# Optimization experiments

Hardware: AMD Instinct MI355X
Metric: run time of the kernel (lower is better)

The kernel has to match this reference:

```python
import jax, jax.numpy as jnp
import numpy as np

B, S, D = 2, 2048, 768
E, TOP_K = 8, 2
H = 4 * D  # expert hidden dim


def setup_inputs() -> dict:
    key = jax.random.key(0)
    ks = jax.random.split(key, 8)
    s_in = 1.0 / np.sqrt(D)
    s_h = 1.0 / np.sqrt(H)
    return {
        "x": jax.random.normal(ks[0], (B, S, D), dtype=jnp.float32),
        "gate_w": jax.random.uniform(ks[1], (D, E), jnp.float32, -s_in, s_in),
        "gate_b": jax.random.uniform(ks[2], (E,), jnp.float32, -s_in, s_in),
        "w1": jax.random.uniform(ks[3], (E, D, H), jnp.float32, -s_in, s_in),
        "b1": jax.random.uniform(ks[4], (E, H), jnp.float32, -s_in, s_in),
        "w2": jax.random.uniform(ks[5], (E, H, D), jnp.float32, -s_h, s_h),
        "b2": jax.random.uniform(ks[6], (E, D), jnp.float32, -s_h, s_h),
    }


def reference(x, gate_w, gate_b, w1, b1, w2, b2):
    # Router: gate linear -> top-k -> softmax over the k selected logits
    logits = jnp.einsum("bsd,de->bse", x, gate_w) + gate_b          # [B,S,E]
    top_vals, top_idx = jax.lax.top_k(logits, TOP_K)                 # [B,S,K]
    rw = jax.nn.softmax(top_vals, axis=-1)                           # [B,S,K]
    # Per-token per-expert combine weight (0 for unselected experts)
    onehot = jax.nn.one_hot(top_idx, E, dtype=x.dtype)               # [B,S,K,E]
    expert_w = jnp.einsum("bske,bsk->bse", onehot, rw)               # [B,S,E]

    # Expert MLPs (GELU exact, matching torch nn.GELU default; dropout is
    # identity in eval). Stacked as grouped GEMMs over the expert axis.
    h = jax.nn.gelu(jnp.einsum("bsd,edh->bseh", x, w1) + b1, approximate=False)
    y = jnp.einsum("bseh,ehd->bsed", h, w2) + b2                     # [B,S,E,D]
    # Weighted combine over experts
    return jnp.einsum("bse,bsed->bsd", expert_w, y)                  # [B,S,D]
```

## Files before the change

### kernel.cpp

```cpp
#include <hip/hip_runtime.h>
#include <hip/hip_bf16.h>

#define D_ 768
#define E_ 8
#define H_ 3072
#define N_TOK 4096
#define BT 64
#define BK 64

typedef _Float16 f16;
typedef f16 f16x8 __attribute__((ext_vector_type(8)));
typedef float f32x4 __attribute__((ext_vector_type(4)));

__device__ __forceinline__ void gld16(const f16* g, f16* l) {
    __builtin_amdgcn_global_load_lds(
        (const __attribute__((address_space(1))) unsigned int*)g,
        (__attribute__((address_space(3))) unsigned int*)l, 16, 0, 0);
}

#define TP 66
__global__ __launch_bounds__(256) void cvt_w_t(const float* __restrict__ in,
                                               f16* __restrict__ outp,
                                               int R, int C) {
    __shared__ f16 t[64][TP];
    const float* src = in + (size_t)blockIdx.z * R * C;
    f16* dst = outp + (size_t)blockIdx.z * R * C;
    int r0 = blockIdx.y * 64, c0 = blockIdx.x * 64;
    int tid = threadIdx.x;
    {
        int r = tid >> 4;
        int c = (tid & 15) * 4;
#pragma unroll
        for (int i = 0; i < 4; i++) {
            float4 v = *(const float4*)(src + (size_t)(r0 + r + i * 16) * C + (c0 + c));
            t[r + i * 16][c] = (f16)v.x;
            t[r + i * 16][c + 1] = (f16)v.y;
            t[r + i * 16][c + 2] = (f16)v.z;
            t[r + i * 16][c + 3] = (f16)v.w;
        }
    }
    __syncthreads();
    {
        int c = tid >> 3;
        int rr = (tid & 7) * 8;
        int ch = rr >> 3;
#pragma unroll
        for (int i = 0; i < 2; i++) {
            int cc = c + i * 32;
            int rowi = c0 + cc;
            f16x8 o;
#pragma unroll
            for (int j = 0; j < 8; j++) o[j] = t[rr + j][cc];
            *(f16x8*)(dst + (size_t)rowi * R + r0 + (((ch ^ rowi) & 7) << 3)) = o;
        }
    }
}

__global__ __launch_bounds__(1024) void router(const float* __restrict__ x,
                                               const float* __restrict__ gw,
                                               const float* __restrict__ gb,
                                               int* __restrict__ counts,
                                               int* __restrict__ list,
                                               float* __restrict__ wslot) {
    __shared__ int lcount[E_];
    __shared__ int lbase[E_];
    __shared__ int te0[64], te1[64], ts0[64], ts1[64];
    __shared__ float tw0[64], tw1[64];

    int tid = threadIdx.x;
    int wv = tid >> 6, lane = tid & 63;
    int s = lane >> 3, eL = lane & 7;
    if (tid < E_) lcount[tid] = 0;
    __syncthreads();

    float biasL = gb[eL];

#pragma unroll 1
    for (int i = 0; i < 4; i++) {
        int lt = wv * 4 + i;
        int tok = blockIdx.x * 64 + lt;
        const float* xr = x + (size_t)tok * D_;
        float a = 0.f;
        const float* gwl = gw + lane;
#pragma unroll 8
        for (int j = 0; j < 96; j++)
            a = fmaf(xr[j * 8 + s], gwl[j * 64], a);
        a += __shfl_xor(a, 8, 64);
        a += __shfl_xor(a, 16, 64);
        a += __shfl_xor(a, 32, 64);
        float lg = a + biasL;
        float le[8];
#pragma unroll
        for (int q = 0; q < 8; q++) le[q] = __shfl(lg, q, 64);
        float v0 = -3.4e38f, v1 = -3.4e38f;
        int i0 = 0, i1 = 0;
#pragma unroll
        for (int q = 0; q < 8; q++) {
            float l = le[q];
            if (l > v0) { v1 = v0; i1 = i0; v0 = l; i0 = q; }
            else if (l > v1) { v1 = l; i1 = q; }
        }
        if (lane == 0) {
            float p1 = expf(v1 - v0);
            float ssum = 1.f + p1;
            int s0 = atomicAdd(&lcount[i0], 1);
            int s1 = atomicAdd(&lcount[i1], 1);
            te0[lt] = i0; ts0[lt] = s0; tw0[lt] = 1.f / ssum;
            te1[lt] = i1; ts1[lt] = s1; tw1[lt] = p1 / ssum;
        }
    }
    __syncthreads();
    if (tid < E_) lbase[tid] = atomicAdd(&counts[tid], lcount[tid]);
    __syncthreads();
    if (tid < 64) {
        int tok = blockIdx.x * 64 + tid;
        int e0 = te0[tid], e1 = te1[tid];
        list[e0 * N_TOK + lbase[e0] + ts0[tid]] = tok * 2;
        list[e1 * N_TOK + lbase[e1] + ts1[tid]] = tok * 2 + 1;
        wslot[tok * 2] = tw0[tid];
        wslot[tok * 2 + 1] = tw1[tid];
    }
}

__global__ void scan8(const int* __restrict__ counts, int* __restrict__ offs) {
    if (threadIdx.x == 0) {
        int s = 0;
#pragma unroll
        for (int e = 0; e < E_; e++) { offs[e] = s; s += counts[e]; }
        offs[E_] = s;
    }
}

__global__ __launch_bounds__(256) void pack_a(const float* __restrict__ x,
                                              const int* __restrict__ counts,
                                              const int* __restrict__ offs,
                                              const int* __restrict__ list,
                                              f16* __restrict__ xg) {
    int wv = threadIdx.x >> 6, lane = threadIdx.x & 63;
    int idx = blockIdx.x * 4 + wv;
    int e = idx >> 12, j = idx & (N_TOK - 1);
    if (j >= counts[e]) return;
    int id = list[idx];
    int row = offs[e] + j;
    const float* xr = x + (size_t)(id >> 1) * D_;
    f16* dst = xg + (size_t)row * D_;
    int r7 = row & 7;
#pragma unroll
    for (int c = 0; c < 3; c++) {
        int h = lane * 4 + c * 256;
        float4 v = *(const float4*)(xr + h);
        f16 o[4] = {(f16)v.x, (f16)v.y, (f16)v.z, (f16)v.w};
        int hs = (h & ~0x3F) | ((((h >> 3) ^ r7) & 7) << 3) | (h & 7);
        *(float2*)(dst + hs) = *(const float2*)o;
    }
}

#define NXB1 (H_ / BT)
__global__ __launch_bounds__(256, 8) void gemm1(const f16* __restrict__ xg,
                                                const f16* __restrict__ w1t,
                                                const float* __restrict__ b1,
                                                const int* __restrict__ counts,
                                                const int* __restrict__ offs,
                                                f16* __restrict__ hbuf) {
    int bid = blockIdx.x;
    int e = bid & 7;
    int r = bid >> 3;
    int xb = r % NXB1;
    int yb = r / NXB1;
    int cnt = counts[e];
    int off = offs[e];
    int rb = yb * BT;
    if (rb >= cnt) return;
    int cb = xb * BT;

    __shared__ f16 lds[2 * BT * BK];
    char* ldsb = (char*)lds;

    int tid = threadIdx.x;
    int wv = tid >> 6, lane = tid & 63;
    int lr = lane >> 3, lc = lane & 7;

    int r0l = wv * 8 + lr;
    int r1l = 32 + wv * 8 + lr;
    int ag0 = off + rb + r0l; if (ag0 > 8191) ag0 = 8191;
    int ag1 = off + rb + r1l; if (ag1 > 8191) ag1 = 8191;
    const f16* ap0 = xg + (size_t)ag0 * D_ + lc * 8;
    const f16* ap1 = xg + (size_t)ag1 * D_ + lc * 8;
    const f16* wb = w1t + (size_t)e * H_ * D_;
    const f16* bp0 = wb + (size_t)(cb + r0l) * D_ + lc * 8;
    const f16* bp1 = wb + (size_t)(cb + r1l) * D_ + lc * 8;
    f16* la0 = lds + wv * 512;
    f16* la1 = lds + 2048 + wv * 512;
    f16* lb0 = lds + 4096 + wv * 512;
    f16* lb1 = lds + 6144 + wv * 512;

    int wr = (wv >> 1) * 32, wc = (wv & 1) * 32;
    int fr = lane & 15, qh = lane >> 4;
    int koff = (off + rb) & 7;

    int roA[2][2], roB[2][2];
#pragma unroll
    for (int m = 0; m < 2; m++)
#pragma unroll
        for (int ks = 0; ks < 2; ks++) {
            int row = wr + m * 16 + fr;
            roA[m][ks] = row * 128 + ((((ks * 4 + qh) ^ (koff + row)) & 7) << 4);
            int rwb = wc + m * 16 + fr;
            roB[m][ks] = 8192 + rwb * 128 + ((((ks * 4 + qh) ^ rwb) & 7) << 4);
        }

    f32x4 acc[2][2] = {};
    const int NT = D_ / BK;
#pragma unroll 1
    for (int t = 0; t < NT; ++t) {
        int kk = t * BK;
        gld16(ap0 + kk, la0);
        gld16(ap1 + kk, la1);
        gld16(bp0 + kk, lb0);
        gld16(bp1 + kk, lb1);
        __syncthreads();
#pragma unroll
        for (int ks = 0; ks < 2; ks++) {
            f16x8 a0 = *(const f16x8*)(ldsb + roA[0][ks]);
            f16x8 a1 = *(const f16x8*)(ldsb + roA[1][ks]);
            f16x8 b0 = *(const f16x8*)(ldsb + roB[0][ks]);
            f16x8 b1v = *(const f16x8*)(ldsb + roB[1][ks]);
            acc[0][0] = __builtin_amdgcn_mfma_f32_16x16x32_f16(a0, b0, acc[0][0], 0, 0, 0);
            acc[0][1] = __builtin_amdgcn_mfma_f32_16x16x32_f16(a0, b1v, acc[0][1], 0, 0, 0);
            acc[1][0] = __builtin_amdgcn_mfma_f32_16x16x32_f16(a1, b0, acc[1][0], 0, 0, 0);
            acc[1][1] = __builtin_amdgcn_mfma_f32_16x16x32_f16(a1, b1v, acc[1][1], 0, 0, 0);
        }
        __syncthreads();
    }

#pragma unroll
    for (int n = 0; n < 2; n++) {
        int colg = cb + wc + n * 16 + fr;
        float bias = b1[e * H_ + colg];
#pragma unroll
        for (int m = 0; m < 2; m++) {
#pragma unroll
            for (int r2 = 0; r2 < 4; r2++) {
                int j = rb + wr + m * 16 + qh * 4 + r2;
                if (j < cnt) {
                    float v = acc[m][n][r2] + bias;
                    v = 0.5f * v * (1.f + erff(v * 0.70710678f));
                    int row = off + j;
                    int hs = (colg & ~0x3F) | ((((colg >> 3) ^ row) & 7) << 3) | (colg & 7);
                    hbuf[(size_t)row * H_ + hs] = (f16)v;
                }
            }
        }
    }
}

#define KSPLIT 2
#define KCH (H_ / KSPLIT)
#define NXB2 ((D_ / BT) * KSPLIT)
__global__ __launch_bounds__(256, 8) void gemm2(const f16* __restrict__ hbuf,
                                                const f16* __restrict__ w2t,
                                                const float* __restrict__ b2,
                                                const int* __restrict__ counts,
                                                const int* __restrict__ offs,
                                                const int* __restrict__ list,
                                                const float* __restrict__ wslot,
                                                float* __restrict__ out) {
    int bid = blockIdx.x;
    int e = bid & 7;
    int r = bid >> 3;
    int xk = r % NXB2;
    int yb = r / NXB2;
    int cnt = counts[e];
    int off = offs[e];
    int rb = yb * BT;
    if (rb >= cnt) return;
    int cb = (xk % (D_ / BT)) * BT;
    int kz = xk / (D_ / BT);
    int k0 = kz * KCH;

    __shared__ f16 lds[2 * BT * BK];
    char* ldsb = (char*)lds;

    int tid = threadIdx.x;
    int wv = tid >> 6, lane = tid & 63;
    int lr = lane >> 3, lc = lane & 7;

    int r0l = wv * 8 + lr;
    int r1l = 32 + wv * 8 + lr;
    int ag0 = off + rb + r0l; if (ag0 > 8191) ag0 = 8191;
    int ag1 = off + rb + r1l; if (ag1 > 8191) ag1 = 8191;
    const f16* ap0 = hbuf + (size_t)ag0 * H_ + k0 + lc * 8;
    const f16* ap1 = hbuf + (size_t)ag1 * H_ + k0 + lc * 8;
    const f16* wb = w2t + (size_t)e * D_ * H_;
    const f16* bp0 = wb + (size_t)(cb + r0l) * H_ + k0 + lc * 8;
    const f16* bp1 = wb + (size_t)(cb + r1l) * H_ + k0 + lc * 8;
    f16* la0 = lds + wv * 512;
    f16* la1 = lds + 2048 + wv * 512;
    f16* lb0 = lds + 4096 + wv * 512;
    f16* lb1 = lds + 6144 + wv * 512;

    int wr = (wv >> 1) * 32, wc = (wv & 1) * 32;
    int fr = lane & 15, qh = lane >> 4;
    int koff = (off + rb) & 7;

    int roA[2][2], roB[2][2];
#pragma unroll
    for (int m = 0; m < 2; m++)
#pragma unroll
        for (int ks = 0; ks < 2; ks++) {
            int row = wr + m * 16 + fr;
            roA[m][ks] = row * 128 + ((((ks * 4 + qh) ^ (koff + row)) & 7) << 4);
            int rwb = wc + m * 16 + fr;
            roB[m][ks] = 8192 + rwb * 128 + ((((ks * 4 + qh) ^ rwb) & 7) << 4);
        }

    f32x4 acc[2][2] = {};
    const int NT = KCH / BK;
#pragma unroll 1
    for (int t = 0; t < NT; ++t) {
        int kk = t * BK;
        gld16(ap0 + kk, la0);
        gld16(ap1 + kk, la1);
        gld16(bp0 + kk, lb0);
        gld16(bp1 + kk, lb1);
        __syncthreads();
#pragma unroll
        for (int ks = 0; ks < 2; ks++) {
            f16x8 a0 = *(const f16x8*)(ldsb + roA[0][ks]);
            f16x8 a1 = *(const f16x8*)(ldsb + roA[1][ks]);
            f16x8 b0 = *(const f16x8*)(ldsb + roB[0][ks]);
            f16x8 b1v = *(const f16x8*)(ldsb + roB[1][ks]);
            acc[0][0] = __builtin_amdgcn_mfma_f32_16x16x32_f16(a0, b0, acc[0][0], 0, 0, 0);
            acc[0][1] = __builtin_amdgcn_mfma_f32_16x16x32_f16(a0, b1v, acc[0][1], 0, 0, 0);
            acc[1][0] = __builtin_amdgcn_mfma_f32_16x16x32_f16(a1, b0, acc[1][0], 0, 0, 0);
            acc[1][1] = __builtin_amdgcn_mfma_f32_16x16x32_f16(a1, b1v, acc[1][1], 0, 0, 0);
        }
        __syncthreads();
    }

#pragma unroll
    for (int n = 0; n < 2; n++) {
        int colg = cb + wc + n * 16 + fr;
        float bias = (kz == 0) ? b2[e * D_ + colg] : 0.f;
#pragma unroll
        for (int m = 0; m < 2; m++) {
#pragma unroll
            for (int r2 = 0; r2 < 4; r2++) {
                int j = rb + wr + m * 16 + qh * 4 + r2;
                if (j < cnt) {
                    int id = list[e * N_TOK + j];
                    float w = wslot[id];
                    float v = (acc[m][n][r2] + bias) * w;
                    atomicAdd(&out[(size_t)(id >> 1) * D_ + colg], v);
                }
            }
        }
    }
}

extern "C" void kernel_launch(void* const* d_in, const int* in_sizes, int n_in,
                              void* d_out, int out_size, void* d_ws, size_t ws_size,
                              hipStream_t stream) {
    const float* x = (const float*)d_in[0];
    const float* gate_w = (const float*)d_in[1];
    const float* gate_b = (const float*)d_in[2];
    const float* w1 = (const float*)d_in[3];
    const float* b1 = (const float*)d_in[4];
    const float* w2 = (const float*)d_in[5];
    const float* b2 = (const float*)d_in[6];
    float* out = (float*)d_out;

    char* ws = (char*)d_ws;
    int* counts = (int*)ws;
    int* offs = (int*)(ws + 256);
    int* list = (int*)(ws + 1024);
    float* wslot = (float*)(ws + 132096);
    f16* xg = (f16*)(ws + 196608);
    f16* w1t = (f16*)(ws + 12779520);
    f16* w2t = (f16*)(ws + 50528256);
    f16* hbuf = (f16*)(ws + 88276992);

    hipMemsetAsync(counts, 0, 256, stream);
    hipMemsetAsync(out, 0, (size_t)out_size * sizeof(float), stream);

    router<<<64, 1024, 0, stream>>>(x, gate_w, gate_b, counts, list, wslot);
    scan8<<<1, 64, 0, stream>>>(counts, offs);
    pack_a<<<E_ * N_TOK / 4, 256, 0, stream>>>(x, counts, offs, list, xg);
    cvt_w_t<<<dim3(H_ / 64, D_ / 64, E_), 256, 0, stream>>>(w1, w1t, D_, H_);
    cvt_w_t<<<dim3(D_ / 64, H_ / 64, E_), 256, 0, stream>>>(w2, w2t, H_, D_);
    gemm1<<<E_ * NXB1 * (N_TOK / BT), 256, 0, stream>>>(xg, w1t, b1, counts, offs, hbuf);
    gemm2<<<E_ * NXB2 * (N_TOK / BT), 256, 0, stream>>>(hbuf, w2t, b2, counts, offs, list, wslot, out);
}
```

Baseline: 263.3 us.

## Drop scan kernel, merge weight conversions, reorder GEMM block grid

Removes the single-thread scan8 launch by having each kernel compute its expert's offset inline from the counts array. The two weight transpose/convert launches are merged into one kernel that picks w1 or w2 by blockIdx.z. The GEMM block-index decomposition is reordered so consecutive blocks share column tiles across row blocks, which may improve weight-tile cache reuse. Together these cut launch count and serialization gaps, at the cost of a small redundant prefix sum in every block.

```diff
diff --git a/kernel.cpp b/kernel.cpp
--- a/kernel.cpp
+++ b/kernel.cpp
@@ -18,14 +18,34 @@
         (__attribute__((address_space(3))) unsigned int*)l, 16, 0, 0);
 }
 
-#define TP 66
-__global__ __launch_bounds__(256) void cvt_w_t(const float* __restrict__ in,
-                                               f16* __restrict__ outp,
-                                               int R, int C) {
-    __shared__ f16 t[64][TP];
-    const float* src = in + (size_t)blockIdx.z * R * C;
-    f16* dst = outp + (size_t)blockIdx.z * R * C;
-    int r0 = blockIdx.y * 64, c0 = blockIdx.x * 64;
+__device__ __forceinline__ int prefix_off(const int* counts, int e, int* cnt_out) {
+    int off = 0, cnt = 0;
+#pragma unroll
+    for (int q = 0; q < E_; q++) {
+        int cq = counts[q];
+        if (q < e) off += cq;
+        if (q == e) cnt = cq;
+    }
+    *cnt_out = cnt;
+    return off;
+}
+
+__global__ __launch_bounds__(256) void cvt_w_both(const float* __restrict__ w1,
+                                                  const float* __restrict__ w2,
+                                                  f16* __restrict__ w1t,
+                                                  f16* __restrict__ w2t) {
+    __shared__ f16 t[64][66];
+    int z = blockIdx.z;
+    const float* src; f16* dst; int R, C, xb, yb;
+    int bx = blockIdx.x;
+    if (z < E_) {
+        src = w1 + (size_t)z * D_ * H_; dst = w1t + (size_t)z * D_ * H_;
+        R = D_; C = H_; xb = bx % 48; yb = bx / 48;
+    } else {
+        src = w2 + (size_t)(z - E_) * H_ * D_; dst = w2t + (size_t)(z - E_) * H_ * D_;
+        R = H_; C = D_; xb = bx % 12; yb = bx / 12;
+    }
+    int r0 = yb * 64, c0 = xb * 64;
     int tid = threadIdx.x;
     {
         int r = tid >> 4;
@@ -122,26 +142,18 @@
     }
 }
 
-__global__ void scan8(const int* __restrict__ counts, int* __restrict__ offs) {
-    if (threadIdx.x == 0) {
-        int s = 0;
-#pragma unroll
-        for (int e = 0; e < E_; e++) { offs[e] = s; s += counts[e]; }
-        offs[E_] = s;
-    }
-}
-
 __global__ __launch_bounds__(256) void pack_a(const float* __restrict__ x,
                                               const int* __restrict__ counts,
-                                              const int* __restrict__ offs,
                                               const int* __restrict__ list,
                                               f16* __restrict__ xg) {
     int wv = threadIdx.x >> 6, lane = threadIdx.x & 63;
     int idx = blockIdx.x * 4 + wv;
     int e = idx >> 12, j = idx & (N_TOK - 1);
-    if (j >= counts[e]) return;
+    int cnt;
+    int off = prefix_off(counts, e, &cnt);
+    if (j >= cnt) return;
     int id = list[idx];
-    int row = offs[e] + j;
+    int row = off + j;
     const float* xr = x + (size_t)(id >> 1) * D_;
     f16* dst = xg + (size_t)row * D_;
     int r7 = row & 7;
@@ -155,23 +167,22 @@
     }
 }
 
-#define NXB1 (H_ / BT)
 __global__ __launch_bounds__(256, 8) void gemm1(const f16* __restrict__ xg,
                                                 const f16* __restrict__ w1t,
                                                 const float* __restrict__ b1,
                                                 const int* __restrict__ counts,
-                                                const int* __restrict__ offs,
                                                 f16* __restrict__ hbuf) {
     int bid = blockIdx.x;
     int e = bid & 7;
     int r = bid >> 3;
-    int xb = r % NXB1;
-    int yb = r / NXB1;
-    int cnt = counts[e];
-    int off = offs[e];
+    int xb24 = r % 24;
+    int yb = (r / 24) % 64;
+    int xh = r / (24 * 64);
+    int cnt;
+    int off = prefix_off(counts, e, &cnt);
     int rb = yb * BT;
     if (rb >= cnt) return;
-    int cb = xb * BT;
+    int cb = (xh * 24 + xb24) * BT;
 
     __shared__ f16 lds[2 * BT * BK];
     char* ldsb = (char*)lds;
@@ -256,26 +267,24 @@
 
 #define KSPLIT 2
 #define KCH (H_ / KSPLIT)
-#define NXB2 ((D_ / BT) * KSPLIT)
 __global__ __launch_bounds__(256, 8) void gemm2(const f16* __restrict__ hbuf,
                                                 const f16* __restrict__ w2t,
                                                 const float* __restrict__ b2,
                                                 const int* __restrict__ counts,
-                                                const int* __restrict__ offs,
                                                 const int* __restrict__ list,
                                                 const float* __restrict__ wslot,
                                                 float* __restrict__ out) {
     int bid = blockIdx.x;
     int e = bid & 7;
     int r = bid >> 3;
-    int xk = r % NXB2;
-    int yb = r / NXB2;
-    int cnt = counts[e];
-    int off = offs[e];
+    int cb12 = r % 12;
+    int yb = (r / 12) % 64;
+    int kz = r / (12 * 64);
+    int cnt;
+    int off = prefix_off(counts, e, &cnt);
     int rb = yb * BT;
     if (rb >= cnt) return;
-    int cb = (xk % (D_ / BT)) * BT;
-    int kz = xk / (D_ / BT);
+    int cb = cb12 * BT;
     int k0 = kz * KCH;
 
     __shared__ f16 lds[2 * BT * BK];
@@ -372,7 +381,6 @@
 
     char* ws = (char*)d_ws;
     int* counts = (int*)ws;
-    int* offs = (int*)(ws + 256);
     int* list = (int*)(ws + 1024);
     float* wslot = (float*)(ws + 132096);
     f16* xg = (f16*)(ws + 196608);
@@ -384,10 +392,8 @@
     hipMemsetAsync(out, 0, (size_t)out_size * sizeof(float), stream);
 
     router<<<64, 1024, 0, stream>>>(x, gate_w, gate_b, counts, list, wslot);
-    scan8<<<1, 64, 0, stream>>>(counts, offs);
-    pack_a<<<E_ * N_TOK / 4, 256, 0, stream>>>(x, counts, offs, list, xg);
-    cvt_w_t<<<dim3(H_ / 64, D_ / 64, E_), 256, 0, stream>>>(w1, w1t, D_, H_);
-    cvt_w_t<<<dim3(D_ / 64, H_ / 64, E_), 256, 0, stream>>>(w2, w2t, H_, D_);
-    gemm1<<<E_ * NXB1 * (N_TOK / BT), 256, 0, stream>>>(xg, w1t, b1, counts, offs, hbuf);
-    gemm2<<<E_ * NXB2 * (N_TOK / BT), 256, 0, stream>>>(hbuf, w2t, b2, counts, offs, list, wslot, out);
-}
+    pack_a<<<E_ * N_TOK / 4, 256, 0, stream>>>(x, counts, list, xg);
+    cvt_w_both<<<dim3(576, 1, 16), 256, 0, stream>>>(w1, w2, w1t, w2t);
+    gemm1<<<E_ * 2 * 64 * 24, 256, 0, stream>>>(xg, w1t, b1, counts, hbuf);
+    gemm2<<<E_ * 2 * 64 * 12, 256, 0, stream>>>(hbuf, w2t, b2, counts, list, wslot, out);
+}
```

Measured after the change: 252.8 us. -4.0%, faster.
